# Optimization experiments

Hardware: AMD Instinct MI355X
Metric: run time of the kernel (lower is better)

Reference implementation:

```python
import jax, jax.numpy as jnp
import numpy as np

NODE_NUMS = 128
IN_SIZE = 256
OUT_SIZE = 256
BATCH = 4096


def setup_inputs() -> dict:
    key = jax.random.key(0)
    k1, k2, k3, k4, k5 = jax.random.split(key, 5)
    # Xavier-uniform bounds
    limit_w = float(np.sqrt(6.0 / (IN_SIZE + OUT_SIZE)))
    limit_b = float(np.sqrt(6.0 / (NODE_NUMS + OUT_SIZE)))
    x = jax.random.normal(k1, (BATCH, IN_SIZE), dtype=jnp.float32)
    var_vector = jax.random.normal(k2, (BATCH, 16), dtype=jnp.float32)  # unused in forward
    W_1 = jax.random.uniform(k3, (NODE_NUMS, IN_SIZE, OUT_SIZE), dtype=jnp.float32,
                             minval=-limit_w, maxval=limit_w)
    b_1 = jax.random.uniform(k4, (NODE_NUMS, OUT_SIZE), dtype=jnp.float32,
                             minval=-limit_b, maxval=limit_b)
    node_ind = jax.random.randint(k5, (2, BATCH), 0, NODE_NUMS, dtype=jnp.int32)
    return {"x": x, "var_vector": var_vector, "W_1": W_1, "b_1": b_1, "node_ind": node_ind}


def reference(x, var_vector, W_1, b_1, node_ind):
    # idx selects a per-sample expert (node) weight matrix and bias.
    idx = node_ind[1]                       # [B]
    W = W_1[idx]                            # [B, in, out] gathered weights
    b = b_1[idx]                            # [B, out]
    # bmm(x[:,None,:], W).squeeze() + b  ==  einsum over the input dim
    return jnp.einsum('bi,bio->bo', x, W) + b
```

## Files before the change

kernel.cpp:

```cpp
#include <hip/hip_runtime.h>

#define BATCH 4096
#define INS   256
#define OUTS  256
#define NODES 128
#define NT    64
#define MCH   32
#define PITCH 264

typedef short short8 __attribute__((ext_vector_type(8)));
typedef float f32x4  __attribute__((ext_vector_type(4)));

struct SMem {
    unsigned short wt[NT * PITCH];
    unsigned short xs[MCH * PITCH];
    unsigned short list[BATCH];
    int cnt;
};

__device__ __forceinline__ unsigned short f2bf(float f) {
    unsigned int u = __builtin_bit_cast(unsigned int, f);
    u += 0x7fffu + ((u >> 16) & 1u);
    return (unsigned short)(u >> 16);
}

__global__ __launch_bounds__(256, 2) void moe_fwd(
    const float* __restrict__ x, const float* __restrict__ W1,
    const float* __restrict__ b1, const int* __restrict__ nid,
    float* __restrict__ out)
{
    __shared__ SMem sm;
    const int t   = threadIdx.x;
    const int bid = blockIdx.x;
    const int e  = (bid & 7) * 16 + ((bid >> 3) >> 2);
    const int c0 = ((bid >> 3) & 3) * NT;

    if (t == 0) sm.cnt = 0;
    __syncthreads();

    const int* __restrict__ idxp = nid + BATCH;
    #pragma unroll
    for (int it = 0; it < BATCH / 256; ++it) {
        int b = it * 256 + t;
        if (idxp[b] == e) {
            int p = atomicAdd(&sm.cnt, 1);
            sm.list[p] = (unsigned short)b;
        }
    }
    __syncthreads();
    const int cnt = sm.cnt;
    if (cnt == 0) return;

    const float* __restrict__ wgp = W1 + (size_t)e * (INS * OUTS) + c0;
    #pragma unroll
    for (int it = 0; it < (NT * 32) / 256; ++it) {
        int idx = it * 256 + t;
        int c   = idx & (NT - 1);
        int kb  = idx >> 6;
        short8 v;
        #pragma unroll
        for (int j = 0; j < 8; ++j) {
            float f = wgp[(size_t)(kb * 8 + j) * OUTS + c];
            v[j] = (short)f2bf(f);
        }
        *reinterpret_cast<short8*>(&sm.wt[c * PITCH + kb * 8]) = v;
    }

    const int w  = t >> 6;
    const int l  = t & 63;
    const int g  = l >> 4;
    const int ln = l & 15;
    const float bval = b1[e * OUTS + c0 + w * 16 + ln];
    const int cc = c0 + w * 16 + ln;

    for (int m0 = 0; m0 < cnt; m0 += MCH) {
        if (m0 > 0) __syncthreads();
        #pragma unroll
        for (int it = 0; it < (MCH * 64) / 256; ++it) {
            int idx = it * 256 + t;
            int k4  = idx & 63;
            int r   = idx >> 6;
            uint2 p = make_uint2(0u, 0u);
            int rr = m0 + r;
            if (rr < cnt) {
                int s = sm.list[rr];
                const float4 vv = *reinterpret_cast<const float4*>(
                    x + (size_t)s * INS + k4 * 4);
                unsigned int lo = (unsigned int)f2bf(vv.x) | ((unsigned int)f2bf(vv.y) << 16);
                unsigned int hi = (unsigned int)f2bf(vv.z) | ((unsigned int)f2bf(vv.w) << 16);
                p = make_uint2(lo, hi);
            }
            *reinterpret_cast<uint2*>(&sm.xs[r * PITCH + k4 * 4]) = p;
        }
        __syncthreads();

        f32x4 acc0 = {0.f, 0.f, 0.f, 0.f};
        f32x4 acc1 = {0.f, 0.f, 0.f, 0.f};
        #pragma unroll
        for (int ks = 0; ks < 8; ++ks) {
            short8 a0 = *reinterpret_cast<const short8*>(
                &sm.xs[ln * PITCH + ks * 32 + g * 8]);
            short8 a1 = *reinterpret_cast<const short8*>(
                &sm.xs[(16 + ln) * PITCH + ks * 32 + g * 8]);
            short8 bb = *reinterpret_cast<const short8*>(
                &sm.wt[(w * 16 + ln) * PITCH + ks * 32 + g * 8]);
            acc0 = __builtin_amdgcn_mfma_f32_16x16x32_bf16(a0, bb, acc0, 0, 0, 0);
            acc1 = __builtin_amdgcn_mfma_f32_16x16x32_bf16(a1, bb, acc1, 0, 0, 0);
        }

        #pragma unroll
        for (int q = 0; q < 4; ++q) {
            int r0 = m0 + g * 4 + q;
            if (r0 < cnt)
                out[(size_t)sm.list[r0] * OUTS + cc] = acc0[q] + bval;
            int r1 = m0 + 16 + g * 4 + q;
            if (r1 < cnt)
                out[(size_t)sm.list[r1] * OUTS + cc] = acc1[q] + bval;
        }
    }
}

extern "C" void kernel_launch(void* const* d_in, const int* in_sizes, int n_in,
                              void* d_out, int out_size, void* d_ws, size_t ws_size,
                              hipStream_t stream) {
    const float* x   = (const float*)d_in[0];
    const float* W1  = (const float*)d_in[2];
    const float* b1  = (const float*)d_in[3];
    const int*   nid = (const int*)d_in[4];
    float* out = (float*)d_out;

    hipLaunchKernelGGL(moe_fwd, dim3(NODES * (OUTS / NT)), dim3(256), 0, stream,
                       x, W1, b1, nid, out);
}
```

Measured before the change: 24.26 us.

## Keep expert weights in registers and load x fragments directly from global

Each lane now loads its own slice of the expert's weight column into registers, issued before the routing scan so the loads overlap it, and converts them to bf16 MFMA fragments kept in registers. The weight and x tiles no longer go through LDS, and x rows are read straight from global per lane. This removes most LDS traffic and the per-chunk barriers, so occupancy is raised to 4 blocks per CU. The costs are many more registers per thread and uncoalesced strided global loads for both W and x.

```diff
diff --git a/kernel.cpp b/kernel.cpp
--- a/kernel.cpp
+++ b/kernel.cpp
@@ -6,14 +6,11 @@
 #define NODES 128
 #define NT    64
 #define MCH   32
-#define PITCH 264
 
 typedef short short8 __attribute__((ext_vector_type(8)));
 typedef float f32x4  __attribute__((ext_vector_type(4)));
 
 struct SMem {
-    unsigned short wt[NT * PITCH];
-    unsigned short xs[MCH * PITCH];
     unsigned short list[BATCH];
     int cnt;
 };
@@ -24,7 +21,16 @@
     return (unsigned short)(u >> 16);
 }
 
-__global__ __launch_bounds__(256, 2) void moe_fwd(
+__device__ __forceinline__ short8 pack8(float4 a, float4 b) {
+    short8 r;
+    r[0] = (short)f2bf(a.x); r[1] = (short)f2bf(a.y);
+    r[2] = (short)f2bf(a.z); r[3] = (short)f2bf(a.w);
+    r[4] = (short)f2bf(b.x); r[5] = (short)f2bf(b.y);
+    r[6] = (short)f2bf(b.z); r[7] = (short)f2bf(b.w);
+    return r;
+}
+
+__global__ __launch_bounds__(256, 4) void moe_fwd(
     const float* __restrict__ x, const float* __restrict__ W1,
     const float* __restrict__ b1, const int* __restrict__ nid,
     float* __restrict__ out)
@@ -35,8 +41,24 @@
     const int e  = (bid & 7) * 16 + ((bid >> 3) >> 2);
     const int c0 = ((bid >> 3) & 3) * NT;
 
+    const int w  = t >> 6;
+    const int l  = t & 63;
+    const int g  = l >> 4;
+    const int ln = l & 15;
+    const int cc = c0 + w * 16 + ln;
+
     if (t == 0) sm.cnt = 0;
     __syncthreads();
+
+    const float* __restrict__ wp = W1 + (size_t)e * (INS * OUTS) + cc;
+    float wraw[64];
+    #pragma unroll
+    for (int ks = 0; ks < 8; ++ks) {
+        #pragma unroll
+        for (int j = 0; j < 8; ++j)
+            wraw[ks * 8 + j] = wp[(size_t)(ks * 32 + g * 8 + j) * OUTS];
+    }
+    const float bval = b1[e * OUTS + cc];
 
     const int* __restrict__ idxp = nid + BATCH;
     #pragma unroll
@@ -47,75 +69,52 @@
             sm.list[p] = (unsigned short)b;
         }
     }
-    __syncthreads();
+    asm volatile("s_waitcnt lgkmcnt(0)" ::: "memory");
+    __builtin_amdgcn_s_barrier();
+    asm volatile("" ::: "memory");
+
     const int cnt = sm.cnt;
     if (cnt == 0) return;
 
-    const float* __restrict__ wgp = W1 + (size_t)e * (INS * OUTS) + c0;
+    short8 wf[8];
     #pragma unroll
-    for (int it = 0; it < (NT * 32) / 256; ++it) {
-        int idx = it * 256 + t;
-        int c   = idx & (NT - 1);
-        int kb  = idx >> 6;
+    for (int ks = 0; ks < 8; ++ks) {
         short8 v;
         #pragma unroll
-        for (int j = 0; j < 8; ++j) {
-            float f = wgp[(size_t)(kb * 8 + j) * OUTS + c];
-            v[j] = (short)f2bf(f);
-        }
-        *reinterpret_cast<short8*>(&sm.wt[c * PITCH + kb * 8]) = v;
+        for (int j = 0; j < 8; ++j) v[j] = (short)f2bf(wraw[ks * 8 + j]);
+        wf[ks] = v;
     }
 
-    const int w  = t >> 6;
-    const int l  = t & 63;
-    const int g  = l >> 4;
-    const int ln = l & 15;
-    const float bval = b1[e * OUTS + c0 + w * 16 + ln];
-    const int cc = c0 + w * 16 + ln;
-
     for (int m0 = 0; m0 < cnt; m0 += MCH) {
-        if (m0 > 0) __syncthreads();
-        #pragma unroll
-        for (int it = 0; it < (MCH * 64) / 256; ++it) {
-            int idx = it * 256 + t;
-            int k4  = idx & 63;
-            int r   = idx >> 6;
-            uint2 p = make_uint2(0u, 0u);
-            int rr = m0 + r;
-            if (rr < cnt) {
-                int s = sm.list[rr];
-                const float4 vv = *reinterpret_cast<const float4*>(
-                    x + (size_t)s * INS + k4 * 4);
-                unsigned int lo = (unsigned int)f2bf(vv.x) | ((unsigned int)f2bf(vv.y) << 16);
-                unsigned int hi = (unsigned int)f2bf(vv.z) | ((unsigned int)f2bf(vv.w) << 16);
-                p = make_uint2(lo, hi);
-            }
-            *reinterpret_cast<uint2*>(&sm.xs[r * PITCH + k4 * 4]) = p;
-        }
-        __syncthreads();
+        int r0 = m0 + ln;
+        int r1 = m0 + 16 + ln;
+        int s0 = sm.list[r0 < cnt ? r0 : cnt - 1];
+        int s1 = sm.list[r1 < cnt ? r1 : cnt - 1];
+        const float* __restrict__ xp0 = x + (size_t)s0 * INS + g * 8;
+        const float* __restrict__ xp1 = x + (size_t)s1 * INS + g * 8;
 
         f32x4 acc0 = {0.f, 0.f, 0.f, 0.f};
         f32x4 acc1 = {0.f, 0.f, 0.f, 0.f};
         #pragma unroll
         for (int ks = 0; ks < 8; ++ks) {
-            short8 a0 = *reinterpret_cast<const short8*>(
-                &sm.xs[ln * PITCH + ks * 32 + g * 8]);
-            short8 a1 = *reinterpret_cast<const short8*>(
-                &sm.xs[(16 + ln) * PITCH + ks * 32 + g * 8]);
-            short8 bb = *reinterpret_cast<const short8*>(
-                &sm.wt[(w * 16 + ln) * PITCH + ks * 32 + g * 8]);
-            acc0 = __builtin_amdgcn_mfma_f32_16x16x32_bf16(a0, bb, acc0, 0, 0, 0);
-            acc1 = __builtin_amdgcn_mfma_f32_16x16x32_bf16(a1, bb, acc1, 0, 0, 0);
+            float4 u0 = *reinterpret_cast<const float4*>(xp0 + ks * 32);
+            float4 u1 = *reinterpret_cast<const float4*>(xp0 + ks * 32 + 4);
+            float4 v0 = *reinterpret_cast<const float4*>(xp1 + ks * 32);
+            float4 v1 = *reinterpret_cast<const float4*>(xp1 + ks * 32 + 4);
+            short8 a0 = pack8(u0, u1);
+            short8 a1 = pack8(v0, v1);
+            acc0 = __builtin_amdgcn_mfma_f32_16x16x32_bf16(a0, wf[ks], acc0, 0, 0, 0);
+            acc1 = __builtin_amdgcn_mfma_f32_16x16x32_bf16(a1, wf[ks], acc1, 0, 0, 0);
         }
 
         #pragma unroll
         for (int q = 0; q < 4; ++q) {
-            int r0 = m0 + g * 4 + q;
-            if (r0 < cnt)
-                out[(size_t)sm.list[r0] * OUTS + cc] = acc0[q] + bval;
-            int r1 = m0 + 16 + g * 4 + q;
-            if (r1 < cnt)
-                out[(size_t)sm.list[r1] * OUTS + cc] = acc1[q] + bval;
+            int rr0 = m0 + g * 4 + q;
+            if (rr0 < cnt)
+                out[(size_t)sm.list[rr0] * OUTS + cc] = acc0[q] + bval;
+            int rr1 = m0 + 16 + g * 4 + q;
+            if (rr1 < cnt)
+                out[(size_t)sm.list[rr1] * OUTS + cc] = acc1[q] + bval;
         }
     }
 }
```

Result: slower. 25.41 us (+4.8%).
